# Kernel optimization log

Measured on AMD Instinct MI355X. Metric: run time of the kernel, lower is better.

## Reference

```python
import jax, jax.numpy as jnp
import numpy as np

N, E = 100000, 1600000
HID, EDIM, TDIM = 64, 16, 32
EIN = 2 * HID + EDIM + 1 + TDIM  # 177
NIN = 2 * HID + TDIM             # 160


def _lin(key, fan_in, fan_out, bias=True):
    k1, k2 = jax.random.split(key)
    lim = 1.0 / np.sqrt(fan_in)
    W = jax.random.uniform(k1, (fan_in, fan_out), jnp.float32, -lim, lim)
    if bias:
        b = jax.random.uniform(k2, (fan_out,), jnp.float32, -lim, lim)
        return W, b
    return W


def setup_inputs() -> dict:
    key = jax.random.key(0)
    ks = jax.random.split(key, 16)
    h = jax.random.normal(ks[0], (N, HID), jnp.float32)
    pos = jax.random.normal(ks[1], (N, 3), jnp.float32)
    edge_index = jax.random.randint(ks[2], (2, E), 0, N, jnp.int64)
    edge_attr = jax.random.normal(ks[3], (E, EDIM), jnp.float32)
    task_emb = jax.random.normal(ks[4], (N, TDIM), jnp.float32)
    ew1, eb1 = _lin(ks[5], EIN, HID)
    ew2, eb2 = _lin(ks[6], HID, HID)
    nw1, nb1 = _lin(ks[7], NIN, HID)
    nw2, nb2 = _lin(ks[8], HID, HID)
    cw1, cb1 = _lin(ks[9], HID, HID)
    cw2 = _lin(ks[10], HID, 1, bias=False)
    sw, sb = _lin(ks[11], TDIM, HID)
    tw, tb = _lin(ks[12], TDIM, HID)
    return dict(h=h, pos=pos, edge_attr=edge_attr, task_emb=task_emb,
                edge_index=edge_index,
                ew1=ew1, eb1=eb1, ew2=ew2, eb2=eb2,
                nw1=nw1, nb1=nb1, nw2=nw2, nb2=nb2,
                cw1=cw1, cb1=cb1, cw2=cw2,
                sw=sw, sb=sb, tw=tw, tb=tb)


def reference(h, pos, edge_attr, task_emb, edge_index,
              ew1, eb1, ew2, eb2, nw1, nb1, nw2, nb2,
              cw1, cb1, cw2, sw, sb, tw, tb):
    row, col = edge_index[0], edge_index[1]
    # gather endpoint features
    rel_pos = pos[row] - pos[col]                      # [E,3]
    dist = jnp.linalg.norm(rel_pos, axis=1, keepdims=True)  # [E,1]
    edge_input = jnp.concatenate([h[row], h[col], edge_attr, dist, task_emb[row]], axis=1)
    m_ij = jax.nn.silu(jax.nn.silu(edge_input @ ew1 + eb1) @ ew2 + eb2)  # [E,HID]
    # scatter-add messages to destination nodes
    m_i = jax.ops.segment_sum(m_ij, col, num_segments=h.shape[0])        # [N,HID]
    node_input = jnp.concatenate([h, m_i, task_emb], axis=1)
    h_update = jax.nn.silu(node_input @ nw1 + nb1) @ nw2 + nb2
    # FiLM task conditioning
    h_update = (task_emb @ sw + sb) * h_update + (task_emb @ tw + tb)
    h_new = h + h_update
    # equivariant coordinate update
    coord_weights = jax.nn.silu(m_ij @ cw1 + cb1) @ cw2                  # [E,1]
    coord_diff = coord_weights * rel_pos / (dist + 1e-08)
    pos_update = jax.ops.segment_sum(coord_diff, col, num_segments=pos.shape[0])
    pos_new = pos + pos_update
    return (h_new, pos_new)
```

## Files before the change

### kernel.cpp

```cpp
#include <hip/hip_runtime.h>
#include <math.h>

#define NN 100000
#define EE 1600000
#define HID 64
#define EDIM 16
#define TDIM 32

__device__ __forceinline__ float silu_f(float x) {
    const float e = __expf(-x);
    return x * __builtin_amdgcn_rcpf(1.0f + e);
}

__device__ __forceinline__ void fma4(float* acc, const float4 x, const float* __restrict__ w) {
#pragma unroll
    for (int j = 0; j < HID; ++j)
        acc[j] += x.x * w[j] + x.y * w[HID + j] + x.z * w[2 * HID + j] + x.w * w[3 * HID + j];
}

__global__ void __launch_bounds__(256)
init_kernel(const float* __restrict__ pos, float* __restrict__ m_i,
            float* __restrict__ pos_out)
{
    const int i = blockIdx.x * 256 + threadIdx.x;
    const float4 z = make_float4(0.f, 0.f, 0.f, 0.f);
    if (i < NN * HID / 4) reinterpret_cast<float4*>(m_i)[i] = z;
    if (i < NN * 3 / 4)
        reinterpret_cast<float4*>(pos_out)[i] = reinterpret_cast<const float4*>(pos)[i];
}

__global__ void __launch_bounds__(256)
edge_kernel(const float* __restrict__ h, const float* __restrict__ pos,
            const float* __restrict__ ea, const float* __restrict__ te,
            const int* __restrict__ ei,
            const float* __restrict__ ew1, const float* __restrict__ eb1,
            const float* __restrict__ ew2, const float* __restrict__ eb2,
            const float* __restrict__ cw1, const float* __restrict__ cb1,
            const float* __restrict__ cw2,
            float* __restrict__ m_i, float* __restrict__ pos_out)
{
    const int e = blockIdx.x * 256 + threadIdx.x;
    if (e >= EE) return;
    const int row = ei[e];
    const int col = ei[EE + e];

    const float rx = pos[3 * row + 0] - pos[3 * col + 0];
    const float ry = pos[3 * row + 1] - pos[3 * col + 1];
    const float rz = pos[3 * row + 2] - pos[3 * col + 2];
    const float dist = sqrtf(rx * rx + ry * ry + rz * rz);

    float acc[HID];
#pragma unroll
    for (int j = 0; j < HID; ++j) acc[j] = eb1[j];

    const float4* hr = reinterpret_cast<const float4*>(h + (size_t)row * HID);
#pragma unroll 1
    for (int c = 0; c < 16; ++c) fma4(acc, hr[c], ew1 + (size_t)(c * 4) * HID);

    const float4* hc = reinterpret_cast<const float4*>(h + (size_t)col * HID);
#pragma unroll 1
    for (int c = 0; c < 16; ++c) fma4(acc, hc[c], ew1 + (size_t)(64 + c * 4) * HID);

    const float4* eav = reinterpret_cast<const float4*>(ea + (size_t)e * EDIM);
#pragma unroll 1
    for (int c = 0; c < 4; ++c) fma4(acc, eav[c], ew1 + (size_t)(128 + c * 4) * HID);

    {
        const float* w = ew1 + (size_t)144 * HID;
#pragma unroll
        for (int j = 0; j < HID; ++j) acc[j] += dist * w[j];
    }

    const float4* tev = reinterpret_cast<const float4*>(te + (size_t)row * TDIM);
#pragma unroll 1
    for (int c = 0; c < 8; ++c) fma4(acc, tev[c], ew1 + (size_t)(145 + c * 4) * HID);

    float t[HID];
#pragma unroll
    for (int j = 0; j < HID; ++j) t[j] = silu_f(acc[j]);

    float acc2[HID];
#pragma unroll
    for (int j = 0; j < HID; ++j) acc2[j] = eb2[j];
#pragma unroll
    for (int k = 0; k < HID; ++k) {
        const float x = t[k];
        const float* w = ew2 + (size_t)k * HID;
#pragma unroll
        for (int j = 0; j < HID; ++j) acc2[j] += x * w[j];
    }
#pragma unroll
    for (int j = 0; j < HID; ++j) t[j] = silu_f(acc2[j]);

    float* mdst = m_i + (size_t)col * HID;
#pragma unroll
    for (int j = 0; j < HID; ++j) unsafeAtomicAdd(mdst + j, t[j]);

#pragma unroll
    for (int j = 0; j < HID; ++j) acc2[j] = cb1[j];
#pragma unroll
    for (int k = 0; k < HID; ++k) {
        const float x = t[k];
        const float* w = cw1 + (size_t)k * HID;
#pragma unroll
        for (int j = 0; j < HID; ++j) acc2[j] += x * w[j];
    }
    float cwt = 0.0f;
#pragma unroll
    for (int j = 0; j < HID; ++j) cwt += silu_f(acc2[j]) * cw2[j];

    const float s = cwt / (dist + 1e-8f);
    unsafeAtomicAdd(&pos_out[3 * col + 0], s * rx);
    unsafeAtomicAdd(&pos_out[3 * col + 1], s * ry);
    unsafeAtomicAdd(&pos_out[3 * col + 2], s * rz);
}

__global__ void __launch_bounds__(256)
node_kernel(const float* __restrict__ h, const float* __restrict__ te,
            const float* __restrict__ m_i,
            const float* __restrict__ nw1, const float* __restrict__ nb1,
            const float* __restrict__ nw2, const float* __restrict__ nb2,
            const float* __restrict__ sw, const float* __restrict__ sb,
            const float* __restrict__ tw, const float* __restrict__ tb,
            float* __restrict__ h_out)
{
    const int i = blockIdx.x * 256 + threadIdx.x;
    if (i >= NN) return;

    float acc[HID];
#pragma unroll
    for (int j = 0; j < HID; ++j) acc[j] = nb1[j];

    const float4* hv = reinterpret_cast<const float4*>(h + (size_t)i * HID);
#pragma unroll 1
    for (int c = 0; c < 16; ++c) fma4(acc, hv[c], nw1 + (size_t)(c * 4) * HID);
    const float4* mv = reinterpret_cast<const float4*>(m_i + (size_t)i * HID);
#pragma unroll 1
    for (int c = 0; c < 16; ++c) fma4(acc, mv[c], nw1 + (size_t)(64 + c * 4) * HID);
    const float4* tv = reinterpret_cast<const float4*>(te + (size_t)i * TDIM);
#pragma unroll 1
    for (int c = 0; c < 8; ++c) fma4(acc, tv[c], nw1 + (size_t)(128 + c * 4) * HID);

    float t[HID];
#pragma unroll
    for (int j = 0; j < HID; ++j) t[j] = silu_f(acc[j]);

    float hu[HID];
#pragma unroll
    for (int j = 0; j < HID; ++j) hu[j] = nb2[j];
#pragma unroll
    for (int k = 0; k < HID; ++k) {
        const float x = t[k];
        const float* w = nw2 + (size_t)k * HID;
#pragma unroll
        for (int j = 0; j < HID; ++j) hu[j] += x * w[j];
    }

#pragma unroll
    for (int j = 0; j < HID; ++j) acc[j] = sb[j];
#pragma unroll 1
    for (int c = 0; c < 8; ++c) fma4(acc, tv[c], sw + (size_t)(c * 4) * HID);
#pragma unroll
    for (int j = 0; j < HID; ++j) hu[j] *= acc[j];

#pragma unroll
    for (int j = 0; j < HID; ++j) acc[j] = tb[j];
#pragma unroll 1
    for (int c = 0; c < 8; ++c) fma4(acc, tv[c], tw + (size_t)(c * 4) * HID);

    float4* outv = reinterpret_cast<float4*>(h_out + (size_t)i * HID);
#pragma unroll
    for (int c = 0; c < 16; ++c) {
        const float4 hx = hv[c];
        float4 o;
        o.x = hx.x + hu[4 * c + 0] + acc[4 * c + 0];
        o.y = hx.y + hu[4 * c + 1] + acc[4 * c + 1];
        o.z = hx.z + hu[4 * c + 2] + acc[4 * c + 2];
        o.w = hx.w + hu[4 * c + 3] + acc[4 * c + 3];
        outv[c] = o;
    }
}

extern "C" void kernel_launch(void* const* d_in, const int* in_sizes, int n_in,
                              void* d_out, int out_size, void* d_ws, size_t ws_size,
                              hipStream_t stream)
{
    const float* h    = (const float*)d_in[0];
    const float* pos  = (const float*)d_in[1];
    const float* ea   = (const float*)d_in[2];
    const float* te   = (const float*)d_in[3];
    const int*   ei   = (const int*)d_in[4];
    const float* ew1  = (const float*)d_in[5];
    const float* eb1  = (const float*)d_in[6];
    const float* ew2  = (const float*)d_in[7];
    const float* eb2  = (const float*)d_in[8];
    const float* nw1  = (const float*)d_in[9];
    const float* nb1  = (const float*)d_in[10];
    const float* nw2  = (const float*)d_in[11];
    const float* nb2  = (const float*)d_in[12];
    const float* cw1  = (const float*)d_in[13];
    const float* cb1  = (const float*)d_in[14];
    const float* cw2  = (const float*)d_in[15];
    const float* sw   = (const float*)d_in[16];
    const float* sb   = (const float*)d_in[17];
    const float* tw   = (const float*)d_in[18];
    const float* tb   = (const float*)d_in[19];

    float* h_out   = (float*)d_out;
    float* pos_out = (float*)d_out + (size_t)NN * HID;
    float* m_i     = (float*)d_ws;

    init_kernel<<<(NN * HID / 4 + 255) / 256, 256, 0, stream>>>(pos, m_i, pos_out);

    edge_kernel<<<EE / 256, 256, 0, stream>>>(h, pos, ea, te, ei,
                                              ew1, eb1, ew2, eb2,
                                              cw1, cb1, cw2,
                                              m_i, pos_out);

    node_kernel<<<(NN + 255) / 256, 256, 0, stream>>>(h, te, m_i,
                                                      nw1, nb1, nw2, nb2,
                                                      sw, sb, tw, tb, h_out);
}
```

Measured before the change: 6.494 ms.

## Split each edge and node MLP across four lanes with shuffle exchange

Each edge and each node is now processed by four threads, with each thread owning 16 of the 64 hidden outputs. Activations are exchanged through width-4 shuffles for the 64x64 layers, and a shuffle reduction produces the coordinate weight. This cuts per-thread register arrays from 64 to 16 floats to raise occupancy, and adds four times as many threads to launch. The cost is redundant input gathers per lane, plus shuffle overhead.

```diff
diff --git a/kernel.cpp b/kernel.cpp
--- a/kernel.cpp
+++ b/kernel.cpp
@@ -4,18 +4,55 @@
 #define NN 100000
 #define EE 1600000
 #define HID 64
-#define EDIM 16
-#define TDIM 32
+
 
 __device__ __forceinline__ float silu_f(float x) {
     const float e = __expf(-x);
     return x * __builtin_amdgcn_rcpf(1.0f + e);
 }
 
-__device__ __forceinline__ void fma4(float* acc, const float4 x, const float* __restrict__ w) {
-#pragma unroll
-    for (int j = 0; j < HID; ++j)
-        acc[j] += x.x * w[j] + x.y * w[HID + j] + x.z * w[2 * HID + j] + x.w * w[3 * HID + j];
+__device__ __forceinline__ void load16(float* dst, const float* __restrict__ src) {
+#pragma unroll
+    for (int c = 0; c < 4; ++c) {
+        const float4 v = *reinterpret_cast<const float4*>(src + 4 * c);
+        dst[4 * c + 0] = v.x; dst[4 * c + 1] = v.y;
+        dst[4 * c + 2] = v.z; dst[4 * c + 3] = v.w;
+    }
+}
+
+__device__ __forceinline__ void fma16(float* acc, const float x, const float* __restrict__ w) {
+#pragma unroll
+    for (int c = 0; c < 4; ++c) {
+        const float4 v = *reinterpret_cast<const float4*>(w + 4 * c);
+        acc[4 * c + 0] += x * v.x; acc[4 * c + 1] += x * v.y;
+        acc[4 * c + 2] += x * v.z; acc[4 * c + 3] += x * v.w;
+    }
+}
+
+template <int NV>
+__device__ __forceinline__ void seg(float* acc, const float4* __restrict__ xsrc,
+                                    const float* __restrict__ w) {
+#pragma unroll 1
+    for (int c = 0; c < NV; ++c) {
+        const float4 xv = xsrc[c];
+        const float* wr = w + (size_t)(4 * c) * HID;
+        fma16(acc, xv.x, wr);
+        fma16(acc, xv.y, wr + HID);
+        fma16(acc, xv.z, wr + 2 * HID);
+        fma16(acc, xv.w, wr + 3 * HID);
+    }
+}
+
+__device__ __forceinline__ void qgemm16(float* acc, const float* t_local,
+                                        const float* __restrict__ w) {
+#pragma unroll
+    for (int ko = 0; ko < 4; ++ko) {
+#pragma unroll
+        for (int ki = 0; ki < 16; ++ki) {
+            const float x = __shfl(t_local[ki], ko, 4);
+            fma16(acc, x, w + (size_t)(ko * 16 + ki) * HID);
+        }
+    }
 }
 
 __global__ void __launch_bounds__(256)
@@ -39,8 +76,11 @@
             const float* __restrict__ cw2,
             float* __restrict__ m_i, float* __restrict__ pos_out)
 {
-    const int e = blockIdx.x * 256 + threadIdx.x;
-    if (e >= EE) return;
+    const int tid = blockIdx.x * 256 + threadIdx.x;
+    const int e = tid >> 2;
+    const int q = tid & 3;
+    const int j0 = q << 4;
+
     const int row = ei[e];
     const int col = ei[EE + e];
 
@@ -49,70 +89,49 @@
     const float rz = pos[3 * row + 2] - pos[3 * col + 2];
     const float dist = sqrtf(rx * rx + ry * ry + rz * rz);
 
-    float acc[HID];
-#pragma unroll
-    for (int j = 0; j < HID; ++j) acc[j] = eb1[j];
-
-    const float4* hr = reinterpret_cast<const float4*>(h + (size_t)row * HID);
-#pragma unroll 1
-    for (int c = 0; c < 16; ++c) fma4(acc, hr[c], ew1 + (size_t)(c * 4) * HID);
-
-    const float4* hc = reinterpret_cast<const float4*>(h + (size_t)col * HID);
-#pragma unroll 1
-    for (int c = 0; c < 16; ++c) fma4(acc, hc[c], ew1 + (size_t)(64 + c * 4) * HID);
-
-    const float4* eav = reinterpret_cast<const float4*>(ea + (size_t)e * EDIM);
-#pragma unroll 1
-    for (int c = 0; c < 4; ++c) fma4(acc, eav[c], ew1 + (size_t)(128 + c * 4) * HID);
-
-    {
-        const float* w = ew1 + (size_t)144 * HID;
-#pragma unroll
-        for (int j = 0; j < HID; ++j) acc[j] += dist * w[j];
-    }
-
-    const float4* tev = reinterpret_cast<const float4*>(te + (size_t)row * TDIM);
-#pragma unroll 1
-    for (int c = 0; c < 8; ++c) fma4(acc, tev[c], ew1 + (size_t)(145 + c * 4) * HID);
-
-    float t[HID];
-#pragma unroll
-    for (int j = 0; j < HID; ++j) t[j] = silu_f(acc[j]);
-
-    float acc2[HID];
-#pragma unroll
-    for (int j = 0; j < HID; ++j) acc2[j] = eb2[j];
-#pragma unroll
-    for (int k = 0; k < HID; ++k) {
-        const float x = t[k];
-        const float* w = ew2 + (size_t)k * HID;
-#pragma unroll
-        for (int j = 0; j < HID; ++j) acc2[j] += x * w[j];
-    }
-#pragma unroll
-    for (int j = 0; j < HID; ++j) t[j] = silu_f(acc2[j]);
-
-    float* mdst = m_i + (size_t)col * HID;
-#pragma unroll
-    for (int j = 0; j < HID; ++j) unsafeAtomicAdd(mdst + j, t[j]);
-
-#pragma unroll
-    for (int j = 0; j < HID; ++j) acc2[j] = cb1[j];
-#pragma unroll
-    for (int k = 0; k < HID; ++k) {
-        const float x = t[k];
-        const float* w = cw1 + (size_t)k * HID;
-#pragma unroll
-        for (int j = 0; j < HID; ++j) acc2[j] += x * w[j];
-    }
-    float cwt = 0.0f;
-#pragma unroll
-    for (int j = 0; j < HID; ++j) cwt += silu_f(acc2[j]) * cw2[j];
-
-    const float s = cwt / (dist + 1e-8f);
-    unsafeAtomicAdd(&pos_out[3 * col + 0], s * rx);
-    unsafeAtomicAdd(&pos_out[3 * col + 1], s * ry);
-    unsafeAtomicAdd(&pos_out[3 * col + 2], s * rz);
+    float acc[16];
+    load16(acc, eb1 + j0);
+    seg<16>(acc, reinterpret_cast<const float4*>(h + (size_t)row * HID), ew1 + j0);
+    seg<16>(acc, reinterpret_cast<const float4*>(h + (size_t)col * HID),
+            ew1 + (size_t)64 * HID + j0);
+    seg<4>(acc, reinterpret_cast<const float4*>(ea + (size_t)e * 16),
+           ew1 + (size_t)128 * HID + j0);
+    fma16(acc, dist, ew1 + (size_t)144 * HID + j0);
+    seg<8>(acc, reinterpret_cast<const float4*>(te + (size_t)row * 32),
+           ew1 + (size_t)145 * HID + j0);
+
+    float t[16];
+#pragma unroll
+    for (int i = 0; i < 16; ++i) t[i] = silu_f(acc[i]);
+
+    float acc2[16];
+    load16(acc2, eb2 + j0);
+    qgemm16(acc2, t, ew2 + j0);
+    float m[16];
+#pragma unroll
+    for (int i = 0; i < 16; ++i) m[i] = silu_f(acc2[i]);
+
+    float* md = m_i + (size_t)col * HID + j0;
+#pragma unroll
+    for (int i = 0; i < 16; ++i) unsafeAtomicAdd(md + i, m[i]);
+
+    float acc3[16];
+    load16(acc3, cb1 + j0);
+    qgemm16(acc3, m, cw1 + j0);
+
+    float c2[16];
+    load16(c2, cw2 + j0);
+    float part = 0.0f;
+#pragma unroll
+    for (int i = 0; i < 16; ++i) part += silu_f(acc3[i]) * c2[i];
+    part += __shfl_xor(part, 1, 4);
+    part += __shfl_xor(part, 2, 4);
+
+    const float s = part / (dist + 1e-8f);
+    if (q < 3) {
+        const float rc = (q == 0) ? rx : ((q == 1) ? ry : rz);
+        unsafeAtomicAdd(&pos_out[3 * (size_t)col + q], s * rc);
+    }
 }
 
 __global__ void __launch_bounds__(256)
@@ -124,60 +143,48 @@
             const float* __restrict__ tw, const float* __restrict__ tb,
             float* __restrict__ h_out)
 {
-    const int i = blockIdx.x * 256 + threadIdx.x;
-    if (i >= NN) return;
-
-    float acc[HID];
-#pragma unroll
-    for (int j = 0; j < HID; ++j) acc[j] = nb1[j];
-
-    const float4* hv = reinterpret_cast<const float4*>(h + (size_t)i * HID);
-#pragma unroll 1
-    for (int c = 0; c < 16; ++c) fma4(acc, hv[c], nw1 + (size_t)(c * 4) * HID);
-    const float4* mv = reinterpret_cast<const float4*>(m_i + (size_t)i * HID);
-#pragma unroll 1
-    for (int c = 0; c < 16; ++c) fma4(acc, mv[c], nw1 + (size_t)(64 + c * 4) * HID);
-    const float4* tv = reinterpret_cast<const float4*>(te + (size_t)i * TDIM);
-#pragma unroll 1
-    for (int c = 0; c < 8; ++c) fma4(acc, tv[c], nw1 + (size_t)(128 + c * 4) * HID);
-
-    float t[HID];
-#pragma unroll
-    for (int j = 0; j < HID; ++j) t[j] = silu_f(acc[j]);
-
-    float hu[HID];
-#pragma unroll
-    for (int j = 0; j < HID; ++j) hu[j] = nb2[j];
-#pragma unroll
-    for (int k = 0; k < HID; ++k) {
-        const float x = t[k];
-        const float* w = nw2 + (size_t)k * HID;
-#pragma unroll
-        for (int j = 0; j < HID; ++j) hu[j] += x * w[j];
-    }
-
-#pragma unroll
-    for (int j = 0; j < HID; ++j) acc[j] = sb[j];
-#pragma unroll 1
-    for (int c = 0; c < 8; ++c) fma4(acc, tv[c], sw + (size_t)(c * 4) * HID);
-#pragma unroll
-    for (int j = 0; j < HID; ++j) hu[j] *= acc[j];
-
-#pragma unroll
-    for (int j = 0; j < HID; ++j) acc[j] = tb[j];
-#pragma unroll 1
-    for (int c = 0; c < 8; ++c) fma4(acc, tv[c], tw + (size_t)(c * 4) * HID);
-
-    float4* outv = reinterpret_cast<float4*>(h_out + (size_t)i * HID);
-#pragma unroll
-    for (int c = 0; c < 16; ++c) {
-        const float4 hx = hv[c];
+    const int tid = blockIdx.x * 256 + threadIdx.x;
+    const int n = tid >> 2;
+    if (n >= NN) return;
+    const int q = tid & 3;
+    const int j0 = q << 4;
+
+    const float4* tev = reinterpret_cast<const float4*>(te + (size_t)n * 32);
+
+    float acc[16];
+    load16(acc, nb1 + j0);
+    seg<16>(acc, reinterpret_cast<const float4*>(h + (size_t)n * HID), nw1 + j0);
+    seg<16>(acc, reinterpret_cast<const float4*>(m_i + (size_t)n * HID),
+            nw1 + (size_t)64 * HID + j0);
+    seg<8>(acc, tev, nw1 + (size_t)128 * HID + j0);
+
+    float t[16];
+#pragma unroll
+    for (int i = 0; i < 16; ++i) t[i] = silu_f(acc[i]);
+
+    float hu[16];
+    load16(hu, nb2 + j0);
+    qgemm16(hu, t, nw2 + j0);
+
+    float sc[16];
+    load16(sc, sb + j0);
+    seg<8>(sc, tev, sw + j0);
+
+    float sh[16];
+    load16(sh, tb + j0);
+    seg<8>(sh, tev, tw + j0);
+
+    const float* hp = h + (size_t)n * HID + j0;
+    float* op = h_out + (size_t)n * HID + j0;
+#pragma unroll
+    for (int c = 0; c < 4; ++c) {
+        const float4 hx = *reinterpret_cast<const float4*>(hp + 4 * c);
         float4 o;
-        o.x = hx.x + hu[4 * c + 0] + acc[4 * c + 0];
-        o.y = hx.y + hu[4 * c + 1] + acc[4 * c + 1];
-        o.z = hx.z + hu[4 * c + 2] + acc[4 * c + 2];
-        o.w = hx.w + hu[4 * c + 3] + acc[4 * c + 3];
-        outv[c] = o;
+        o.x = hx.x + sc[4 * c + 0] * hu[4 * c + 0] + sh[4 * c + 0];
+        o.y = hx.y + sc[4 * c + 1] * hu[4 * c + 1] + sh[4 * c + 1];
+        o.z = hx.z + sc[4 * c + 2] * hu[4 * c + 2] + sh[4 * c + 2];
+        o.w = hx.w + sc[4 * c + 3] * hu[4 * c + 3] + sh[4 * c + 3];
+        *reinterpret_cast<float4*>(op + 4 * c) = o;
     }
 }
 
@@ -212,12 +219,12 @@
 
     init_kernel<<<(NN * HID / 4 + 255) / 256, 256, 0, stream>>>(pos, m_i, pos_out);
 
-    edge_kernel<<<EE / 256, 256, 0, stream>>>(h, pos, ea, te, ei,
-                                              ew1, eb1, ew2, eb2,
-                                              cw1, cb1, cw2,
-                                              m_i, pos_out);
-
-    node_kernel<<<(NN + 255) / 256, 256, 0, stream>>>(h, te, m_i,
-                                                      nw1, nb1, nw2, nb2,
-                                                      sw, sb, tw, tb, h_out);
-}
+    edge_kernel<<<EE * 4 / 256, 256, 0, stream>>>(h, pos, ea, te, ei,
+                                                  ew1, eb1, ew2, eb2,
+                                                  cw1, cb1, cw2,
+                                                  m_i, pos_out);
+
+    node_kernel<<<(NN * 4 + 255) / 256, 256, 0, stream>>>(h, te, m_i,
+                                                          nw1, nb1, nw2, nb2,
+                                                          sw, sb, tw, tb, h_out);
+}
```

Result: slower. 9.642 ms (+48.5%).

## Stage MLP weights in LDS and use persistent grid-stride edge blocks

Applied to the files above, without the earlier changes.

Edge and node kernels now copy their first and second layer weights and biases into shared memory once per block, then read them as broadcast float4 LDS loads with explicit fmaf instead of scalar global reads. The edge kernel becomes a persistent grid-stride loop over 512 blocks so the weight staging cost is amortised, and both kernels get launch bounds of 2 blocks per CU. The cw1 weights still come from global memory. The roughly 61 KB of LDS per block and the register cap may limit occupancy or cause spills.

```diff
diff --git a/kernel.cpp b/kernel.cpp
--- a/kernel.cpp
+++ b/kernel.cpp
@@ -3,19 +3,36 @@
 
 #define NN 100000
 #define EE 1600000
-#define HID 64
-#define EDIM 16
-#define TDIM 32
+
 
 __device__ __forceinline__ float silu_f(float x) {
     const float e = __expf(-x);
     return x * __builtin_amdgcn_rcpf(1.0f + e);
 }
 
-__device__ __forceinline__ void fma4(float* acc, const float4 x, const float* __restrict__ w) {
-#pragma unroll
-    for (int j = 0; j < HID; ++j)
-        acc[j] += x.x * w[j] + x.y * w[HID + j] + x.z * w[2 * HID + j] + x.w * w[3 * HID + j];
+__device__ __forceinline__ void fmarow(float* acc, const float x, const float* __restrict__ w) {
+#pragma unroll
+    for (int c = 0; c < 16; ++c) {
+        const float4 wv = *reinterpret_cast<const float4*>(w + 4 * c);
+        acc[4 * c + 0] = fmaf(x, wv.x, acc[4 * c + 0]);
+        acc[4 * c + 1] = fmaf(x, wv.y, acc[4 * c + 1]);
+        acc[4 * c + 2] = fmaf(x, wv.z, acc[4 * c + 2]);
+        acc[4 * c + 3] = fmaf(x, wv.w, acc[4 * c + 3]);
+    }
+}
+
+template <int NV>
+__device__ __forceinline__ void seg(float* acc, const float4* __restrict__ xsrc,
+                                    const float* __restrict__ w) {
+#pragma unroll 1
+    for (int c = 0; c < NV; ++c) {
+        const float4 xv = xsrc[c];
+        const float* wr = w + (size_t)(4 * c) * 64;
+        fmarow(acc, xv.x, wr);
+        fmarow(acc, xv.y, wr + 64);
+        fmarow(acc, xv.z, wr + 128);
+        fmarow(acc, xv.w, wr + 192);
+    }
 }
 
 __global__ void __launch_bounds__(256)
@@ -24,12 +41,12 @@
 {
     const int i = blockIdx.x * 256 + threadIdx.x;
     const float4 z = make_float4(0.f, 0.f, 0.f, 0.f);
-    if (i < NN * HID / 4) reinterpret_cast<float4*>(m_i)[i] = z;
+    if (i < NN * 64 / 4) reinterpret_cast<float4*>(m_i)[i] = z;
     if (i < NN * 3 / 4)
         reinterpret_cast<float4*>(pos_out)[i] = reinterpret_cast<const float4*>(pos)[i];
 }
 
-__global__ void __launch_bounds__(256)
+__global__ void __launch_bounds__(256, 2)
 edge_kernel(const float* __restrict__ h, const float* __restrict__ pos,
             const float* __restrict__ ea, const float* __restrict__ te,
             const int* __restrict__ ei,
@@ -39,83 +56,76 @@
             const float* __restrict__ cw2,
             float* __restrict__ m_i, float* __restrict__ pos_out)
 {
-    const int e = blockIdx.x * 256 + threadIdx.x;
-    if (e >= EE) return;
-    const int row = ei[e];
-    const int col = ei[EE + e];
-
-    const float rx = pos[3 * row + 0] - pos[3 * col + 0];
-    const float ry = pos[3 * row + 1] - pos[3 * col + 1];
-    const float rz = pos[3 * row + 2] - pos[3 * col + 2];
-    const float dist = sqrtf(rx * rx + ry * ry + rz * rz);
-
-    float acc[HID];
-#pragma unroll
-    for (int j = 0; j < HID; ++j) acc[j] = eb1[j];
-
-    const float4* hr = reinterpret_cast<const float4*>(h + (size_t)row * HID);
-#pragma unroll 1
-    for (int c = 0; c < 16; ++c) fma4(acc, hr[c], ew1 + (size_t)(c * 4) * HID);
-
-    const float4* hc = reinterpret_cast<const float4*>(h + (size_t)col * HID);
-#pragma unroll 1
-    for (int c = 0; c < 16; ++c) fma4(acc, hc[c], ew1 + (size_t)(64 + c * 4) * HID);
-
-    const float4* eav = reinterpret_cast<const float4*>(ea + (size_t)e * EDIM);
-#pragma unroll 1
-    for (int c = 0; c < 4; ++c) fma4(acc, eav[c], ew1 + (size_t)(128 + c * 4) * HID);
-
+    extern __shared__ float lds[];
+    float* W1 = lds;
+    float* W2 = lds + 11328;
+    float* B  = lds + 15424;
+
+    const int t = threadIdx.x;
     {
-        const float* w = ew1 + (size_t)144 * HID;
-#pragma unroll
-        for (int j = 0; j < HID; ++j) acc[j] += dist * w[j];
-    }
-
-    const float4* tev = reinterpret_cast<const float4*>(te + (size_t)row * TDIM);
-#pragma unroll 1
-    for (int c = 0; c < 8; ++c) fma4(acc, tev[c], ew1 + (size_t)(145 + c * 4) * HID);
-
-    float t[HID];
-#pragma unroll
-    for (int j = 0; j < HID; ++j) t[j] = silu_f(acc[j]);
-
-    float acc2[HID];
-#pragma unroll
-    for (int j = 0; j < HID; ++j) acc2[j] = eb2[j];
-#pragma unroll
-    for (int k = 0; k < HID; ++k) {
-        const float x = t[k];
-        const float* w = ew2 + (size_t)k * HID;
-#pragma unroll
-        for (int j = 0; j < HID; ++j) acc2[j] += x * w[j];
-    }
-#pragma unroll
-    for (int j = 0; j < HID; ++j) t[j] = silu_f(acc2[j]);
-
-    float* mdst = m_i + (size_t)col * HID;
-#pragma unroll
-    for (int j = 0; j < HID; ++j) unsafeAtomicAdd(mdst + j, t[j]);
-
-#pragma unroll
-    for (int j = 0; j < HID; ++j) acc2[j] = cb1[j];
-#pragma unroll
-    for (int k = 0; k < HID; ++k) {
-        const float x = t[k];
-        const float* w = cw1 + (size_t)k * HID;
-#pragma unroll
-        for (int j = 0; j < HID; ++j) acc2[j] += x * w[j];
-    }
-    float cwt = 0.0f;
-#pragma unroll
-    for (int j = 0; j < HID; ++j) cwt += silu_f(acc2[j]) * cw2[j];
-
-    const float s = cwt / (dist + 1e-8f);
-    unsafeAtomicAdd(&pos_out[3 * col + 0], s * rx);
-    unsafeAtomicAdd(&pos_out[3 * col + 1], s * ry);
-    unsafeAtomicAdd(&pos_out[3 * col + 2], s * rz);
-}
-
-__global__ void __launch_bounds__(256)
+        const float4* s1 = reinterpret_cast<const float4*>(ew1);
+        float4* d1 = reinterpret_cast<float4*>(W1);
+        for (int i = t; i < 11328 / 4; i += 256) d1[i] = s1[i];
+        const float4* s2 = reinterpret_cast<const float4*>(ew2);
+        float4* d2 = reinterpret_cast<float4*>(W2);
+        for (int i = t; i < 4096 / 4; i += 256) d2[i] = s2[i];
+        if (t < 64) { B[t] = eb1[t]; B[64 + t] = eb2[t]; B[128 + t] = cb1[t]; B[192 + t] = cw2[t]; }
+    }
+    __syncthreads();
+
+    const int stride = gridDim.x * 256;
+    for (int e = blockIdx.x * 256 + t; e < EE; e += stride) {
+        const int row = ei[e];
+        const int col = ei[EE + e];
+
+        const float rx = pos[3 * row + 0] - pos[3 * col + 0];
+        const float ry = pos[3 * row + 1] - pos[3 * col + 1];
+        const float rz = pos[3 * row + 2] - pos[3 * col + 2];
+        const float dist = sqrtf(rx * rx + ry * ry + rz * rz);
+
+        float acc[64];
+#pragma unroll
+        for (int j = 0; j < 64; ++j) acc[j] = B[j];
+        seg<16>(acc, reinterpret_cast<const float4*>(h + (size_t)row * 64), W1);
+        seg<16>(acc, reinterpret_cast<const float4*>(h + (size_t)col * 64), W1 + 64 * 64);
+        seg<4>(acc, reinterpret_cast<const float4*>(ea + (size_t)e * 16), W1 + 128 * 64);
+        fmarow(acc, dist, W1 + 144 * 64);
+        seg<8>(acc, reinterpret_cast<const float4*>(te + (size_t)row * 32), W1 + 145 * 64);
+
+        float tt[64];
+#pragma unroll
+        for (int j = 0; j < 64; ++j) tt[j] = silu_f(acc[j]);
+
+        float m[64];
+#pragma unroll
+        for (int j = 0; j < 64; ++j) m[j] = B[64 + j];
+#pragma unroll
+        for (int k = 0; k < 64; ++k) fmarow(m, tt[k], W2 + k * 64);
+#pragma unroll
+        for (int j = 0; j < 64; ++j) m[j] = silu_f(m[j]);
+
+        float* md = m_i + (size_t)col * 64;
+#pragma unroll
+        for (int j = 0; j < 64; ++j) unsafeAtomicAdd(md + j, m[j]);
+
+        float a3[64];
+#pragma unroll
+        for (int j = 0; j < 64; ++j) a3[j] = B[128 + j];
+#pragma unroll
+        for (int k = 0; k < 64; ++k) fmarow(a3, m[k], cw1 + (size_t)k * 64);
+
+        float cwt = 0.0f;
+#pragma unroll
+        for (int j = 0; j < 64; ++j) cwt += silu_f(a3[j]) * B[192 + j];
+
+        const float s = cwt / (dist + 1e-8f);
+        unsafeAtomicAdd(&pos_out[3 * (size_t)col + 0], s * rx);
+        unsafeAtomicAdd(&pos_out[3 * (size_t)col + 1], s * ry);
+        unsafeAtomicAdd(&pos_out[3 * (size_t)col + 2], s * rz);
+    }
+}
+
+__global__ void __launch_bounds__(256, 2)
 node_kernel(const float* __restrict__ h, const float* __restrict__ te,
             const float* __restrict__ m_i,
             const float* __restrict__ nw1, const float* __restrict__ nb1,
@@ -124,60 +134,67 @@
             const float* __restrict__ tw, const float* __restrict__ tb,
             float* __restrict__ h_out)
 {
-    const int i = blockIdx.x * 256 + threadIdx.x;
-    if (i >= NN) return;
-
-    float acc[HID];
-#pragma unroll
-    for (int j = 0; j < HID; ++j) acc[j] = nb1[j];
-
-    const float4* hv = reinterpret_cast<const float4*>(h + (size_t)i * HID);
-#pragma unroll 1
-    for (int c = 0; c < 16; ++c) fma4(acc, hv[c], nw1 + (size_t)(c * 4) * HID);
-    const float4* mv = reinterpret_cast<const float4*>(m_i + (size_t)i * HID);
-#pragma unroll 1
-    for (int c = 0; c < 16; ++c) fma4(acc, mv[c], nw1 + (size_t)(64 + c * 4) * HID);
-    const float4* tv = reinterpret_cast<const float4*>(te + (size_t)i * TDIM);
-#pragma unroll 1
-    for (int c = 0; c < 8; ++c) fma4(acc, tv[c], nw1 + (size_t)(128 + c * 4) * HID);
-
-    float t[HID];
-#pragma unroll
-    for (int j = 0; j < HID; ++j) t[j] = silu_f(acc[j]);
-
-    float hu[HID];
-#pragma unroll
-    for (int j = 0; j < HID; ++j) hu[j] = nb2[j];
-#pragma unroll
-    for (int k = 0; k < HID; ++k) {
-        const float x = t[k];
-        const float* w = nw2 + (size_t)k * HID;
-#pragma unroll
-        for (int j = 0; j < HID; ++j) hu[j] += x * w[j];
-    }
-
-#pragma unroll
-    for (int j = 0; j < HID; ++j) acc[j] = sb[j];
-#pragma unroll 1
-    for (int c = 0; c < 8; ++c) fma4(acc, tv[c], sw + (size_t)(c * 4) * HID);
-#pragma unroll
-    for (int j = 0; j < HID; ++j) hu[j] *= acc[j];
-
-#pragma unroll
-    for (int j = 0; j < HID; ++j) acc[j] = tb[j];
-#pragma unroll 1
-    for (int c = 0; c < 8; ++c) fma4(acc, tv[c], tw + (size_t)(c * 4) * HID);
-
-    float4* outv = reinterpret_cast<float4*>(h_out + (size_t)i * HID);
-#pragma unroll
-    for (int c = 0; c < 16; ++c) {
-        const float4 hx = hv[c];
-        float4 o;
-        o.x = hx.x + hu[4 * c + 0] + acc[4 * c + 0];
-        o.y = hx.y + hu[4 * c + 1] + acc[4 * c + 1];
-        o.z = hx.z + hu[4 * c + 2] + acc[4 * c + 2];
-        o.w = hx.w + hu[4 * c + 3] + acc[4 * c + 3];
-        outv[c] = o;
+    extern __shared__ float lds[];
+    float* W1 = lds;
+    float* W2 = lds + 10240;
+    float* B  = lds + 14336;
+
+    const int t = threadIdx.x;
+    {
+        const float4* s1 = reinterpret_cast<const float4*>(nw1);
+        float4* d1 = reinterpret_cast<float4*>(W1);
+        for (int i = t; i < 10240 / 4; i += 256) d1[i] = s1[i];
+        const float4* s2 = reinterpret_cast<const float4*>(nw2);
+        float4* d2 = reinterpret_cast<float4*>(W2);
+        for (int i = t; i < 4096 / 4; i += 256) d2[i] = s2[i];
+        if (t < 64) { B[t] = nb1[t]; B[64 + t] = nb2[t]; B[128 + t] = sb[t]; B[192 + t] = tb[t]; }
+    }
+    __syncthreads();
+
+    const int stride = gridDim.x * 256;
+    for (int n = blockIdx.x * 256 + t; n < NN; n += stride) {
+        const float4* hv = reinterpret_cast<const float4*>(h + (size_t)n * 64);
+        const float4* tev = reinterpret_cast<const float4*>(te + (size_t)n * 32);
+
+        float acc[64];
+#pragma unroll
+        for (int j = 0; j < 64; ++j) acc[j] = B[j];
+        seg<16>(acc, hv, W1);
+        seg<16>(acc, reinterpret_cast<const float4*>(m_i + (size_t)n * 64), W1 + 64 * 64);
+        seg<8>(acc, tev, W1 + 128 * 64);
+
+        float tt[64];
+#pragma unroll
+        for (int j = 0; j < 64; ++j) tt[j] = silu_f(acc[j]);
+
+        float hu[64];
+#pragma unroll
+        for (int j = 0; j < 64; ++j) hu[j] = B[64 + j];
+#pragma unroll
+        for (int k = 0; k < 64; ++k) fmarow(hu, tt[k], W2 + k * 64);
+
+        float f[64];
+#pragma unroll
+        for (int j = 0; j < 64; ++j) f[j] = B[128 + j];
+        seg<8>(f, tev, sw);
+#pragma unroll
+        for (int j = 0; j < 64; ++j) hu[j] *= f[j];
+
+#pragma unroll
+        for (int j = 0; j < 64; ++j) f[j] = B[192 + j];
+        seg<8>(f, tev, tw);
+
+        float* op = h_out + (size_t)n * 64;
+#pragma unroll
+        for (int c = 0; c < 16; ++c) {
+            const float4 hx = hv[c];
+            float4 o;
+            o.x = hx.x + hu[4 * c + 0] + f[4 * c + 0];
+            o.y = hx.y + hu[4 * c + 1] + f[4 * c + 1];
+            o.z = hx.z + hu[4 * c + 2] + f[4 * c + 2];
+            o.w = hx.w + hu[4 * c + 3] + f[4 * c + 3];
+            *reinterpret_cast<float4*>(op + 4 * c) = o;
+        }
     }
 }
 
@@ -207,17 +224,17 @@
     const float* tb   = (const float*)d_in[19];
 
     float* h_out   = (float*)d_out;
-    float* pos_out = (float*)d_out + (size_t)NN * HID;
+    float* pos_out = (float*)d_out + (size_t)NN * 64;
     float* m_i     = (float*)d_ws;
 
-    init_kernel<<<(NN * HID / 4 + 255) / 256, 256, 0, stream>>>(pos, m_i, pos_out);
-
-    edge_kernel<<<EE / 256, 256, 0, stream>>>(h, pos, ea, te, ei,
-                                              ew1, eb1, ew2, eb2,
-                                              cw1, cb1, cw2,
-                                              m_i, pos_out);
-
-    node_kernel<<<(NN + 255) / 256, 256, 0, stream>>>(h, te, m_i,
-                                                      nw1, nb1, nw2, nb2,
-                                                      sw, sb, tw, tb, h_out);
-}
+    init_kernel<<<(NN * 64 / 4 + 255) / 256, 256, 0, stream>>>(pos, m_i, pos_out);
+
+    edge_kernel<<<512, 256, 62720, stream>>>(h, pos, ea, te, ei,
+                                             ew1, eb1, ew2, eb2,
+                                             cw1, cb1, cw2,
+                                             m_i, pos_out);
+
+    node_kernel<<<(NN + 255) / 256, 256, 58368, stream>>>(h, te, m_i,
+                                                          nw1, nb1, nw2, nb2,
+                                                          sw, sb, tw, tb, h_out);
+}
```

Measured after the change: 12.63 ms. +94.5%, slower.
